# Performance work log

Measured on AMD Instinct MI355X. Metric: run time of the kernel, lower is better.

The kernel has to match this reference:

```python
import jax, jax.numpy as jnp
import numpy as np

TWO_PI = 2.0 * np.pi
DIST_THRESH = 0.1  # squared-distance threshold from the source


def _fourier_basis(x, y, K):
    # phase[i, l, k] = 2*pi*(k*x_i + l*y_i), k,l in 1..K, reshaped to [inchans, K*K]
    kk = jnp.arange(1, K + 1, dtype=x.dtype)  # varies along last axis (columns)
    ll = jnp.arange(1, K + 1, dtype=x.dtype)  # varies along middle axis (rows)
    phase = TWO_PI * (kk[None, None, :] * x[:, None, None]
                      + ll[None, :, None] * y[:, None, None])
    phase = phase.reshape(x.shape[0], K * K)
    return jnp.cos(phase), jnp.sin(phase)


def setup_inputs() -> dict:
    key = jax.random.key(0)
    ks = jax.random.split(key, 7)
    B, C_in, C_out, K, T = 128, 273, 270, 32, 2048
    return {
        "X": jax.random.normal(ks[0], (B, C_in, T), dtype=jnp.float32),
        "z_real": jax.random.normal(ks[1], (C_out, K * K), dtype=jnp.float32) / (32.0 * 32.0),
        "z_imag": jax.random.normal(ks[2], (C_out, K * K), dtype=jnp.float32) / (32.0 * 32.0),
        "x": jax.random.uniform(ks[3], (C_in,), dtype=jnp.float32),
        "y": jax.random.uniform(ks[4], (C_in,), dtype=jnp.float32),
        "x_drop": jax.random.uniform(ks[5], (), dtype=jnp.float32),
        "y_drop": jax.random.uniform(ks[6], (), dtype=jnp.float32),
    }


def reference(X, z_real, z_imag, x, y, x_drop, y_drop):
    K = int(np.sqrt(z_real.shape[1]))
    cos_m, sin_m = _fourier_basis(x, y, K)          # [C_in, K*K] each
    # logits over input channels: [C_out, C_in]
    a = z_real @ cos_m.T + z_imag @ sin_m.T
    # zero (not -inf) logits of channels near the drop point, as in the source
    dist2 = (x_drop - x) ** 2 + (y_drop - y) ** 2   # [C_in]
    a = jnp.where((dist2 < DIST_THRESH)[None, :], 0.0, a)
    a = jax.nn.softmax(a, axis=1)                    # [C_out, C_in]
    return jnp.einsum('oi,bit->bot', a, X)           # [B, C_out, T]
```

## Files before the change

kernel.cpp:

```cpp
#include <hip/hip_runtime.h>
#include <hip/hip_bf16.h>
#include <math.h>

typedef short s16x4 __attribute__((ext_vector_type(4)));
typedef short bf16x8 __attribute__((ext_vector_type(8)));
typedef float f32x16 __attribute__((ext_vector_type(16)));

#define C_IN 273
#define C_OUT 270
#define T_DIM 2048
#define KP 288
#define NKS 18

#define XT_KS_STRIDE 65536u
#define XT_PER_B 1179648u
#define WS2_COS   150994944u
#define WS2_SIN   152113152u
#define WS2_PART  153231360u
#define WS2_APERM 155738112u
#define APR2_KS_STRIDE 9216u

__device__ __forceinline__ short f2bf(float f) {
  __hip_bfloat16 h = __float2bfloat16(f);
  short r; __builtin_memcpy(&r, &h, 2); return r;
}

__global__ void k_basis(const float* __restrict__ x, const float* __restrict__ y,
                        float* __restrict__ cosb, float* __restrict__ sinb) {
  const int i = blockIdx.x;
  const float xi = x[i], yi = y[i];
  const int base = threadIdx.x * 4;
  #pragma unroll
  for (int j = 0; j < 4; ++j) {
    const int kl = base + j;
    const float kf = (float)((kl & 31) + 1);
    const float lf = (float)((kl >> 5) + 1);
    const float ph = 6.28318530717958647692f * (kf * xi + lf * yi);
    float sn, cs;
    sincosf(ph, &sn, &cs);
    cosb[(size_t)i * 1024 + kl] = cs;
    sinb[(size_t)i * 1024 + kl] = sn;
  }
}

__global__ __launch_bounds__(256) void k_logits(const float* __restrict__ zr,
    const float* __restrict__ zi, const float* __restrict__ cosb,
    const float* __restrict__ sinb, float* __restrict__ part) {
  const int tx = threadIdx.x & 15, ty = threadIdx.x >> 4;
  const int ibase = blockIdx.x * 64 + tx * 4;
  const int obase = blockIdx.y * 64 + ty * 4;
  const int kl0 = (int)blockIdx.z * 128;
  int oc[4], ic[4];
  #pragma unroll
  for (int a = 0; a < 4; ++a) {
    oc[a] = min(obase + a, C_OUT - 1);
    ic[a] = min(ibase + a, C_IN - 1);
  }
  float acc[4][4] = {};
  for (int kl = kl0; kl < kl0 + 128; kl += 4) {
    float4 zr4[4], zi4[4], cb4[4], sb4[4];
    #pragma unroll
    for (int a = 0; a < 4; ++a) {
      zr4[a] = *(const float4*)(zr + (size_t)oc[a] * 1024 + kl);
      zi4[a] = *(const float4*)(zi + (size_t)oc[a] * 1024 + kl);
    }
    #pragma unroll
    for (int b = 0; b < 4; ++b) {
      cb4[b] = *(const float4*)(cosb + (size_t)ic[b] * 1024 + kl);
      sb4[b] = *(const float4*)(sinb + (size_t)ic[b] * 1024 + kl);
    }
    #pragma unroll
    for (int a = 0; a < 4; ++a)
      #pragma unroll
      for (int b = 0; b < 4; ++b)
        acc[a][b] += zr4[a].x * cb4[b].x + zr4[a].y * cb4[b].y
                   + zr4[a].z * cb4[b].z + zr4[a].w * cb4[b].w
                   + zi4[a].x * sb4[b].x + zi4[a].y * sb4[b].y
                   + zi4[a].z * sb4[b].z + zi4[a].w * sb4[b].w;
  }
  #pragma unroll
  for (int a = 0; a < 4; ++a)
    #pragma unroll
    for (int b = 0; b < 4; ++b) {
      const int o = obase + a, i = ibase + b;
      if (o < C_OUT && i < C_IN)
        part[((size_t)blockIdx.z * 272 + o) * 288 + i] = acc[a][b];
    }
}

__global__ __launch_bounds__(256) void k_softmax(const float* __restrict__ part,
    const float* __restrict__ x, const float* __restrict__ y,
    const float* __restrict__ xdp, const float* __restrict__ ydp,
    __hip_bfloat16* __restrict__ ap2) {
  const int o = blockIdx.x;
  const int tid = threadIdx.x;
  if (o >= C_OUT) {
    for (int s = tid; s < KP; s += 256)
      ap2[(size_t)((s >> 4) * 288 + o) * 16 + (s & 15)] = __float2bfloat16(0.f);
    return;
  }
  __shared__ float red[8];
  const float xd = xdp[0], yd = ydp[0];
  const int i0 = tid, i1 = tid + 256;
  float v0, v1 = 0.f;
  {
    float s = 0.f;
    #pragma unroll
    for (int c = 0; c < 8; ++c) s += part[((size_t)c * 272 + o) * 288 + i0];
    const float dx = xd - x[i0], dy = yd - y[i0];
    v0 = (dx * dx + dy * dy < 0.1f) ? 0.f : s;
  }
  const bool has1 = (i1 < C_IN);
  if (has1) {
    float s = 0.f;
    #pragma unroll
    for (int c = 0; c < 8; ++c) s += part[((size_t)c * 272 + o) * 288 + i1];
    const float dx = xd - x[i1], dy = yd - y[i1];
    v1 = (dx * dx + dy * dy < 0.1f) ? 0.f : s;
  }
  float mv = has1 ? fmaxf(v0, v1) : v0;
  #pragma unroll
  for (int off = 32; off >= 1; off >>= 1) mv = fmaxf(mv, __shfl_down(mv, off));
  if ((tid & 63) == 0) red[tid >> 6] = mv;
  __syncthreads();
  const float M = fmaxf(fmaxf(red[0], red[1]), fmaxf(red[2], red[3]));
  const float e0 = expf(v0 - M);
  const float e1 = has1 ? expf(v1 - M) : 0.f;
  float sv = e0 + e1;
  #pragma unroll
  for (int off = 32; off >= 1; off >>= 1) sv += __shfl_down(sv, off);
  __syncthreads();
  if ((tid & 63) == 0) red[4 + (tid >> 6)] = sv;
  __syncthreads();
  const float S = red[4] + red[5] + red[6] + red[7];
  const float inv = 1.0f / S;
  ap2[(size_t)((i0 >> 4) * 288 + o) * 16 + (i0 & 15)] = __float2bfloat16(e0 * inv);
  if (i1 < KP)
    ap2[(size_t)((i1 >> 4) * 288 + o) * 16 + (i1 & 15)] =
        __float2bfloat16(has1 ? e1 * inv : 0.f);
}

__global__ __launch_bounds__(256) void k_trans(const float* __restrict__ X,
                                               char* __restrict__ Xt) {
  __shared__ __align__(16) char lds[64 * 592];
  const int tid = threadIdx.x;
  const int t0 = blockIdx.x * 64;
  const int b = blockIdx.y;
  const float* Xb = X + (size_t)b * C_IN * T_DIM;
  const int tt = tid & 63, ig = tid >> 6;
  #pragma unroll 4
  for (int p = 0; p < 36; ++p) {
    const int i = p * 8 + ig * 2;
    const float v0 = (i < C_IN) ? Xb[(size_t)i * T_DIM + t0 + tt] : 0.f;
    const float v1 = (i + 1 < C_IN) ? Xb[(size_t)(i + 1) * T_DIM + t0 + tt] : 0.f;
    const unsigned pk = (unsigned)(unsigned short)f2bf(v0)
                      | ((unsigned)(unsigned short)f2bf(v1) << 16);
    *(unsigned*)(lds + tt * 592 + i * 2) = pk;
  }
  __syncthreads();
  char* XtB = Xt + (size_t)b * XT_PER_B;
  #pragma unroll
  for (int j = 0; j < 5; ++j) {
    const int item = j * 256 + tid;
    if (item < NKS * 64) {
      const int tt2 = item & 63, ks = item >> 6;
      const char* src = lds + tt2 * 592 + ks * 32;
      char* dst = XtB + (size_t)ks * XT_KS_STRIDE + (size_t)(t0 + tt2) * 32;
      *(float4*)(dst)      = *(const float4*)(src);
      *(float4*)(dst + 16) = *(const float4*)(src + 16);
    }
  }
}

__global__ __launch_bounds__(256) void k_gemm3(const __hip_bfloat16* __restrict__ ap2,
    const char* __restrict__ Xt, float* __restrict__ out) {
  const int tid = threadIdx.x;
  const int lane = tid & 63, w = tid >> 6;
  const int l32 = lane & 31, lh = lane >> 5;
  const int ob = blockIdx.x;
  const int tb = blockIdx.y;
  const int b  = blockIdx.z;

  const int tblk = tb * 4 + w;
  const char* Bbase = Xt + (size_t)b * XT_PER_B + tblk * 1024 + l32 * 32 + lh * 16;
  const char* Abase = (const char*)ap2 + (ob * 96 + l32) * 32 + lh * 16;

  f32x16 acc[3] = {};
  bf16x8 Bf[3], Af[3][3];

  Bf[0]    = *(const bf16x8*)(Bbase);
  Af[0][0] = *(const bf16x8*)(Abase);
  Af[0][1] = *(const bf16x8*)(Abase + 1024);
  Af[0][2] = *(const bf16x8*)(Abase + 2048);
  Bf[1]    = *(const bf16x8*)(Bbase + XT_KS_STRIDE);
  Af[1][0] = *(const bf16x8*)(Abase + APR2_KS_STRIDE);
  Af[1][1] = *(const bf16x8*)(Abase + APR2_KS_STRIDE + 1024);
  Af[1][2] = *(const bf16x8*)(Abase + APR2_KS_STRIDE + 2048);
  __builtin_amdgcn_sched_barrier(0);

  #pragma unroll
  for (int ks = 0; ks < NKS; ++ks) {
    const int cur = ks % 3;
    if (ks + 2 < NKS) {
      const int nxt = (ks + 2) % 3;
      Bf[nxt]    = *(const bf16x8*)(Bbase + (size_t)(ks + 2) * XT_KS_STRIDE);
      Af[nxt][0] = *(const bf16x8*)(Abase + (ks + 2) * APR2_KS_STRIDE);
      Af[nxt][1] = *(const bf16x8*)(Abase + (ks + 2) * APR2_KS_STRIDE + 1024);
      Af[nxt][2] = *(const bf16x8*)(Abase + (ks + 2) * APR2_KS_STRIDE + 2048);
    }
    __builtin_amdgcn_sched_barrier(0);
    acc[0] = __builtin_amdgcn_mfma_f32_32x32x16_bf16(Af[cur][0], Bf[cur], acc[0], 0, 0, 0);
    acc[1] = __builtin_amdgcn_mfma_f32_32x32x16_bf16(Af[cur][1], Bf[cur], acc[1], 0, 0, 0);
    acc[2] = __builtin_amdgcn_mfma_f32_32x32x16_bf16(Af[cur][2], Bf[cur], acc[2], 0, 0, 0);
    __builtin_amdgcn_sched_barrier(0);
  }

  const int t = tblk * 32 + l32;
  float* outb = out + (size_t)b * C_OUT * T_DIM;
  #pragma unroll
  for (int mi = 0; mi < 3; ++mi)
    #pragma unroll
    for (int r = 0; r < 16; ++r) {
      const int o = ob * 96 + mi * 32 + (r & 3) + 8 * (r >> 2) + 4 * lh;
      if (o < C_OUT)
        outb[(size_t)o * T_DIM + t] = acc[mi][r];
    }
}

extern "C" void kernel_launch(void* const* d_in, const int* in_sizes, int n_in,
                              void* d_out, int out_size, void* d_ws, size_t ws_size,
                              hipStream_t stream) {
  const float* X  = (const float*)d_in[0];
  const float* zr = (const float*)d_in[1];
  const float* zi = (const float*)d_in[2];
  const float* x  = (const float*)d_in[3];
  const float* y  = (const float*)d_in[4];
  const float* xd = (const float*)d_in[5];
  const float* yd = (const float*)d_in[6];
  float* out = (float*)d_out;
  char* ws = (char*)d_ws;

  float* cosb = (float*)(ws + WS2_COS);
  float* sinb = (float*)(ws + WS2_SIN);
  float* part = (float*)(ws + WS2_PART);
  __hip_bfloat16* ap2 = (__hip_bfloat16*)(ws + WS2_APERM);
  char* Xt = ws;

  k_basis<<<dim3(273), dim3(256), 0, stream>>>(x, y, cosb, sinb);
  k_logits<<<dim3(5, 5, 8), dim3(256), 0, stream>>>(zr, zi, cosb, sinb, part);
  k_softmax<<<dim3(KP), dim3(256), 0, stream>>>(part, x, y, xd, yd, ap2);
  k_trans<<<dim3(32, 128), dim3(256), 0, stream>>>(X, Xt);
  k_gemm3<<<dim3(3, 16, 128), dim3(256), 0, stream>>>(ap2, Xt, out);
}
```

Before: 395.1 us.

## Restructure X transpose per k-slab with vectorized loads and XCD-aware GEMM block remap

The transpose kernel now gives each block one 16-channel k-slab across the full T range. It reads rows with coalesced float4 loads, converts them to bf16 into LDS, then writes contiguous 16-byte packed chunks. The GEMM launch becomes a 1D grid whose block index is remapped so that consecutive blocks on the same XCD share batch and tile data, aiming for better L2 locality. Risks are LDS bank conflicts from the 2-byte strided gathers and lower occupancy from the larger LDS footprint.

```diff
diff --git a/kernel.cpp b/kernel.cpp
--- a/kernel.cpp
+++ b/kernel.cpp
@@ -19,6 +19,9 @@
 #define WS2_PART  153231360u
 #define WS2_APERM 155738112u
 #define APR2_KS_STRIDE 9216u
+
+#define TR_ROW 4104
+#define TR_LDS (16 * TR_ROW)
 
 __device__ __forceinline__ short f2bf(float f) {
   __hip_bfloat16 h = __float2bfloat16(f);
@@ -142,33 +145,43 @@
 
 __global__ __launch_bounds__(256) void k_trans(const float* __restrict__ X,
                                                char* __restrict__ Xt) {
-  __shared__ __align__(16) char lds[64 * 592];
+  __shared__ __align__(16) char lds[TR_LDS];
   const int tid = threadIdx.x;
-  const int t0 = blockIdx.x * 64;
-  const int b = blockIdx.y;
+  const int ks = blockIdx.x;
+  const int b  = blockIdx.y;
   const float* Xb = X + (size_t)b * C_IN * T_DIM;
-  const int tt = tid & 63, ig = tid >> 6;
-  #pragma unroll 4
-  for (int p = 0; p < 36; ++p) {
-    const int i = p * 8 + ig * 2;
-    const float v0 = (i < C_IN) ? Xb[(size_t)i * T_DIM + t0 + tt] : 0.f;
-    const float v1 = (i + 1 < C_IN) ? Xb[(size_t)(i + 1) * T_DIM + t0 + tt] : 0.f;
-    const unsigned pk = (unsigned)(unsigned short)f2bf(v0)
-                      | ((unsigned)(unsigned short)f2bf(v1) << 16);
-    *(unsigned*)(lds + tt * 592 + i * 2) = pk;
-  }
-  __syncthreads();
-  char* XtB = Xt + (size_t)b * XT_PER_B;
-  #pragma unroll
-  for (int j = 0; j < 5; ++j) {
-    const int item = j * 256 + tid;
-    if (item < NKS * 64) {
-      const int tt2 = item & 63, ks = item >> 6;
-      const char* src = lds + tt2 * 592 + ks * 32;
-      char* dst = XtB + (size_t)ks * XT_KS_STRIDE + (size_t)(t0 + tt2) * 32;
-      *(float4*)(dst)      = *(const float4*)(src);
-      *(float4*)(dst + 16) = *(const float4*)(src + 16);
-    }
+
+  const int ri = tid >> 4;
+  const int tq = tid & 15;
+  const int gi = ks * 16 + ri;
+  const bool valid = (gi < C_IN);
+  const float* src = Xb + (size_t)gi * T_DIM + tq * 4;
+  char* ldsrow = lds + ri * TR_ROW + tq * 8;
+
+  #pragma unroll 8
+  for (int p = 0; p < 32; ++p) {
+    float4 v = valid ? *(const float4*)(src + p * 64) : make_float4(0.f, 0.f, 0.f, 0.f);
+    s16x4 pk;
+    pk[0] = f2bf(v.x); pk[1] = f2bf(v.y); pk[2] = f2bf(v.z); pk[3] = f2bf(v.w);
+    *(s16x4*)(ldsrow + p * 128) = pk;
+  }
+  __syncthreads();
+
+  char* dstB = Xt + (size_t)b * XT_PER_B + (size_t)ks * XT_KS_STRIDE;
+  #pragma unroll
+  for (int it = 0; it < 16; ++it) {
+    const int u = it * 256 + tid;
+    const int t = u >> 1, half = (u & 1) * 8;
+    unsigned short w[8];
+    #pragma unroll
+    for (int r = 0; r < 8; ++r)
+      w[r] = *(const unsigned short*)(lds + (half + r) * TR_ROW + t * 2);
+    uint4 pk;
+    pk.x = (unsigned)w[0] | ((unsigned)w[1] << 16);
+    pk.y = (unsigned)w[2] | ((unsigned)w[3] << 16);
+    pk.z = (unsigned)w[4] | ((unsigned)w[5] << 16);
+    pk.w = (unsigned)w[6] | ((unsigned)w[7] << 16);
+    *(uint4*)(dstB + (size_t)u * 16) = pk;
   }
 }
 
@@ -177,9 +190,12 @@
   const int tid = threadIdx.x;
   const int lane = tid & 63, w = tid >> 6;
   const int l32 = lane & 31, lh = lane >> 5;
-  const int ob = blockIdx.x;
-  const int tb = blockIdx.y;
-  const int b  = blockIdx.z;
+  const int bid = blockIdx.x;
+  const int L = (bid & 7) * 768 + (bid >> 3);
+  const int ob = L % 3;
+  const int rest = L / 3;
+  const int tb = rest & 15;
+  const int b  = rest >> 4;
 
   const int tblk = tb * 4 + w;
   const char* Bbase = Xt + (size_t)b * XT_PER_B + tblk * 1024 + l32 * 32 + lh * 16;
@@ -249,6 +265,6 @@
   k_basis<<<dim3(273), dim3(256), 0, stream>>>(x, y, cosb, sinb);
   k_logits<<<dim3(5, 5, 8), dim3(256), 0, stream>>>(zr, zi, cosb, sinb, part);
   k_softmax<<<dim3(KP), dim3(256), 0, stream>>>(part, x, y, xd, yd, ap2);
-  k_trans<<<dim3(32, 128), dim3(256), 0, stream>>>(X, Xt);
-  k_gemm3<<<dim3(3, 16, 128), dim3(256), 0, stream>>>(ap2, Xt, out);
-}
+  k_trans<<<dim3(18, 128), dim3(256), 0, stream>>>(X, Xt);
+  k_gemm3<<<dim3(6144), dim3(256), 0, stream>>>(ap2, Xt, out);
+}
```

New measurement: 348.6 us. 11.8% less time.
